# Performance work log

Measured on AMD Instinct MI355X. Metric: run time of the kernel, lower is better.

The kernel has to match this reference:

```python
import jax, jax.numpy as jnp
import numpy as np
import math

N_EMBD = 1024
N_HEAD = 16
B, T = 2, 2048


def new_gelu(x):
    # GPT-2 tanh-approx GELU (matches torch module exactly)
    return 0.5 * x * (1.0 + jnp.tanh(jnp.sqrt(2.0 / jnp.pi) * (x + 0.044715 * x ** 3)))


def layer_norm(x, w, b, eps=1e-5):
    mu = jnp.mean(x, axis=-1, keepdims=True)
    var = jnp.var(x, axis=-1, keepdims=True)
    return (x - mu) * jax.lax.rsqrt(var + eps) * w + b


def setup_inputs() -> dict:
    key = jax.random.key(0)
    ks = jax.random.split(key, 8)
    C = N_EMBD
    s = 0.02
    return {
        "x": jax.random.normal(ks[0], (B, T, C), dtype=jnp.float32),
        "ln1_w": jnp.ones((C,), jnp.float32),
        "ln1_b": jnp.zeros((C,), jnp.float32),
        "attn_w": s * jax.random.normal(ks[1], (C, 3 * C), jnp.float32),
        "attn_b": jnp.zeros((3 * C,), jnp.float32),
        "attn_proj_w": s * jax.random.normal(ks[2], (C, C), jnp.float32),
        "attn_proj_b": jnp.zeros((C,), jnp.float32),
        "ln2_w": jnp.ones((C,), jnp.float32),
        "ln2_b": jnp.zeros((C,), jnp.float32),
        "fc_w": s * jax.random.normal(ks[3], (C, 4 * C), jnp.float32),
        "fc_b": jnp.zeros((4 * C,), jnp.float32),
        "mlp_proj_w": s * jax.random.normal(ks[4], (4 * C, C), jnp.float32),
        "mlp_proj_b": jnp.zeros((C,), jnp.float32),
    }


def block_forward(x, ln1_w, ln1_b, attn_w, attn_b, attn_proj_w, attn_proj_b,
                  ln2_w, ln2_b, fc_w, fc_b, mlp_proj_w, mlp_proj_b):
    Bm, Tm, C = x.shape
    H = N_HEAD
    D = C // H
    # --- self attention (pre-LN) ---
    h = layer_norm(x, ln1_w, ln1_b)
    qkv = h @ attn_w + attn_b  # [B,T,3C]
    q, k, v = jnp.split(qkv, 3, axis=-1)
    q = q.reshape(Bm, Tm, H, D).transpose(0, 2, 1, 3)  # [B,H,T,D]
    k = k.reshape(Bm, Tm, H, D).transpose(0, 2, 1, 3)
    v = v.reshape(Bm, Tm, H, D).transpose(0, 2, 1, 3)
    att = jnp.einsum('bhqd,bhkd->bhqk', q, k) * (1.0 / math.sqrt(D))
    att = jax.nn.softmax(att, axis=-1)  # NOTE: no causal mask in source
    y = jnp.einsum('bhqk,bhkd->bhqd', att, v)
    y = y.transpose(0, 2, 1, 3).reshape(Bm, Tm, C)
    x = x + (y @ attn_proj_w + attn_proj_b)
    # --- MLP ---
    h = layer_norm(x, ln2_w, ln2_b)
    h = new_gelu(h @ fc_w + fc_b)
    x = x + (h @ mlp_proj_w + mlp_proj_b)
    return x


def reference(x, ln1_w, ln1_b, attn_w, attn_b, attn_proj_w, attn_proj_b,
              ln2_w, ln2_b, fc_w, fc_b, mlp_proj_w, mlp_proj_b):
    return block_forward(x, ln1_w, ln1_b, attn_w, attn_b, attn_proj_w, attn_proj_b,
                         ln2_w, ln2_b, fc_w, fc_b, mlp_proj_w, mlp_proj_b)
```

## Files before the change

### kernel.cpp

```cpp
#include <hip/hip_runtime.h>

typedef __attribute__((ext_vector_type(4))) float  f32x4;
typedef __attribute__((ext_vector_type(8))) short  s16x8;
typedef __attribute__((ext_vector_type(4))) short  s16x4;

__device__ __forceinline__ short f2bf(float f) {
    unsigned u = __builtin_bit_cast(unsigned, f);
    u += 0x7fff + ((u >> 16) & 1);
    return (short)(u >> 16);
}

__device__ __forceinline__ void load_lds16(const void* g, void* l) {
    __builtin_amdgcn_global_load_lds(
        (const __attribute__((address_space(1))) unsigned int*)g,
        (__attribute__((address_space(3))) unsigned int*)l, 16, 0, 0);
}

__global__ __launch_bounds__(256) void transpose_cast(const float* __restrict__ W,
                                                      short* __restrict__ Wt,
                                                      int K, int N) {
    __shared__ float t[32][33];
    int n0 = blockIdx.x * 32, k0 = blockIdx.y * 32;
    int tx = threadIdx.x & 31, ty = threadIdx.x >> 5;
#pragma unroll
    for (int i = 0; i < 4; i++)
        t[ty + 8 * i][tx] = W[(size_t)(k0 + ty + 8 * i) * N + n0 + tx];
    __syncthreads();
#pragma unroll
    for (int i = 0; i < 4; i++)
        Wt[(size_t)(n0 + ty + 8 * i) * K + k0 + tx] = f2bf(t[tx][ty + 8 * i]);
}

__global__ __launch_bounds__(256) void vtrans_kernel(const short* __restrict__ qkv,
                                                     short* __restrict__ Vtg) {
    const int T = 2048, C3 = 3072;
    __shared__ short tl[32][33];
    int bh = blockIdx.y >> 1;
    int b = bh >> 4, h = bh & 15;
    int dh = (blockIdx.y & 1) * 32;
    int t0 = blockIdx.x * 32;
    int tx = threadIdx.x & 31, ty = threadIdx.x >> 5;
    const short* src = qkv + (size_t)b * T * C3 + 2048 + h * 64 + dh;
#pragma unroll
    for (int i = 0; i < 4; i++)
        tl[ty + 8 * i][tx] = src[(size_t)(t0 + ty + 8 * i) * C3 + tx];
    __syncthreads();
#pragma unroll
    for (int i = 0; i < 4; i++)
        Vtg[((size_t)bh * 64 + dh + ty + 8 * i) * T + t0 + tx] = tl[tx][ty + 8 * i];
}

__global__ __launch_bounds__(256) void ln_kernel(const float* __restrict__ x,
                                                 const float* __restrict__ w,
                                                 const float* __restrict__ b,
                                                 short* __restrict__ out) {
    int row = blockIdx.x;
    int tid = threadIdx.x;
    const float4 v = ((const float4*)(x + (size_t)row * 1024))[tid];
    float s  = v.x + v.y + v.z + v.w;
    float ss = v.x * v.x + v.y * v.y + v.z * v.z + v.w * v.w;
#pragma unroll
    for (int o = 32; o > 0; o >>= 1) {
        s  += __shfl_down(s, o);
        ss += __shfl_down(ss, o);
    }
    __shared__ float rs[4], rq[4];
    int wave = tid >> 6, lane = tid & 63;
    if (lane == 0) { rs[wave] = s; rq[wave] = ss; }
    __syncthreads();
    float tot = rs[0] + rs[1] + rs[2] + rs[3];
    float tq  = rq[0] + rq[1] + rq[2] + rq[3];
    float mu   = tot * (1.f / 1024.f);
    float var  = tq * (1.f / 1024.f) - mu * mu;
    float rstd = rsqrtf(var + 1e-5f);
    const float4 wv = ((const float4*)w)[tid];
    const float4 bv = ((const float4*)b)[tid];
    s16x4 o;
    o[0] = f2bf((v.x - mu) * rstd * wv.x + bv.x);
    o[1] = f2bf((v.y - mu) * rstd * wv.y + bv.y);
    o[2] = f2bf((v.z - mu) * rstd * wv.z + bv.z);
    o[3] = f2bf((v.w - mu) * rstd * wv.w + bv.w);
    ((s16x4*)(out + (size_t)row * 1024))[tid] = o;
}

template <typename OUT_T, bool GELU, bool RES, bool SCALE_Q>
__global__ __launch_bounds__(256) void gemm_bt(const short* __restrict__ A,
                                               const short* __restrict__ Bt,
                                               const float* __restrict__ bias,
                                               const float* __restrict__ res,
                                               OUT_T* __restrict__ C,
                                               int M, int N, int K) {
    __shared__ __align__(16) short As[128 * 32];
    __shared__ __align__(16) short Bs[128 * 32];
    int tid = threadIdx.x;
    int m0 = blockIdx.y * 128, n0 = blockIdx.x * 128;
    int wave = tid >> 6, lane = tid & 63;
    int wr = wave >> 1, wc = wave & 1;
    int g = lane >> 4, q = lane & 15;
    f32x4 acc[4][4] = {};
    const short* Ab = A + (size_t)m0 * K;
    const short* Bb = Bt + (size_t)n0 * K;
    int srow = tid >> 2;
    int scol = (tid & 3) * 8;
    for (int k0 = 0; k0 < K; k0 += 32) {
        __syncthreads();
        load_lds16(Ab + (size_t)srow * K + k0 + scol, As + tid * 8);
        load_lds16(Ab + (size_t)(srow + 64) * K + k0 + scol, As + 2048 + tid * 8);
        load_lds16(Bb + (size_t)srow * K + k0 + scol, Bs + tid * 8);
        load_lds16(Bb + (size_t)(srow + 64) * K + k0 + scol, Bs + 2048 + tid * 8);
        __syncthreads();
        s16x8 a[4], bf[4];
#pragma unroll
        for (int mi = 0; mi < 4; mi++)
            a[mi] = *(const s16x8*)(As + (wr * 64 + mi * 16 + q) * 32 + g * 8);
#pragma unroll
        for (int ni = 0; ni < 4; ni++)
            bf[ni] = *(const s16x8*)(Bs + (wc * 64 + ni * 16 + q) * 32 + g * 8);
#pragma unroll
        for (int mi = 0; mi < 4; mi++)
#pragma unroll
            for (int ni = 0; ni < 4; ni++)
                acc[mi][ni] = __builtin_amdgcn_mfma_f32_16x16x32_bf16(a[mi], bf[ni], acc[mi][ni], 0, 0, 0);
    }
#pragma unroll
    for (int mi = 0; mi < 4; mi++) {
#pragma unroll
        for (int ni = 0; ni < 4; ni++) {
            int row = m0 + wr * 64 + mi * 16 + g * 4;
            int col = n0 + wc * 64 + ni * 16 + q;
            float bb = bias[col];
#pragma unroll
            for (int r = 0; r < 4; r++) {
                float v = acc[mi][ni][r] + bb;
                if (RES) v += res[(size_t)(row + r) * N + col];
                if (GELU) {
                    float aa = 0.7978845608028654f * (v + 0.044715f * v * v * v);
                    float th = 1.f - 2.f / (__expf(2.f * aa) + 1.f);
                    v = 0.5f * v * (1.f + th);
                }
                if (SCALE_Q && col < 1024) v *= 0.18033688011112042f;
                if constexpr (sizeof(OUT_T) == 2)
                    C[(size_t)(row + r) * N + col] = f2bf(v);
                else
                    C[(size_t)(row + r) * N + col] = v;
            }
        }
    }
}

__global__ __launch_bounds__(256) void attn_kernel(const short* __restrict__ qkv,
                                                   const short* __restrict__ Vtg,
                                                   short* __restrict__ y) {
    const int T = 2048, C3 = 3072;
    int wg = blockIdx.x;
    int mapped = (wg & 7) * 128 + (wg >> 3);
    int bh = mapped >> 5, qt = mapped & 31;
    int b = bh >> 4, h = bh & 15;
    int tid = threadIdx.x, lane = tid & 63, wave = tid >> 6;
    int g = lane >> 4, q = lane & 15;
    const short* base = qkv + (size_t)b * T * C3;

    int qrow = qt * 64 + wave * 16 + q;
    const short* qp = base + (size_t)qrow * C3 + h * 64 + g * 8;
    s16x8 qf0 = *(const s16x8*)qp;
    s16x8 qf1 = *(const s16x8*)(qp + 32);

    __shared__ __align__(16) short Ks[2][64 * 64];
    __shared__ __align__(16) short Vs[2][64 * 64];
    __shared__ __align__(16) short Pl[4][16 * 64];

    int srow = tid >> 3, sc8 = tid & 7;
    const short* ksrc = base + 1024 + h * 64 + (size_t)srow * C3 + ((sc8 ^ (srow & 7)) << 3);
    const short* vsrc = Vtg + ((size_t)bh * 64 + srow) * T + ((sc8 ^ (srow & 7)) << 3);

    auto stage = [&](int bi, int t) {
        const short* kp = ksrc + (size_t)(t * 64) * C3;
        load_lds16(kp, &Ks[bi][tid * 8]);
        load_lds16(kp + (size_t)32 * C3, &Ks[bi][tid * 8 + 2048]);
        const short* vp = vsrc + t * 64;
        load_lds16(vp, &Vs[bi][tid * 8]);
        load_lds16(vp + (size_t)32 * T, &Vs[bi][tid * 8 + 2048]);
    };

    float mst = -INFINITY, lst = 0.f;
    f32x4 accy[4] = {};
    int sw = q & 7;
    int s2 = sw << 1;

    stage(0, 0);
    for (int t = 0; t < 32; ++t) {
        int cur = t & 1;
        __syncthreads();
        if (t < 31) stage(cur ^ 1, t + 1);
        f32x4 sc[4];
#pragma unroll
        for (int n = 0; n < 4; n++) {
            const short* kb = &Ks[cur][(16 * n + q) * 64];
            s16x8 kf0 = *(const s16x8*)(kb + ((g ^ sw) << 3));
            s16x8 kf1 = *(const s16x8*)(kb + (((g + 4) ^ sw) << 3));
            f32x4 z = {};
            z = __builtin_amdgcn_mfma_f32_16x16x32_bf16(kf0, qf0, z, 0, 0, 0);
            sc[n] = __builtin_amdgcn_mfma_f32_16x16x32_bf16(kf1, qf1, z, 0, 0, 0);
        }
        float tm = -INFINITY;
#pragma unroll
        for (int n = 0; n < 4; n++)
#pragma unroll
            for (int r = 0; r < 4; r++) tm = fmaxf(tm, sc[n][r]);
        tm = fmaxf(tm, __shfl_xor(tm, 16));
        tm = fmaxf(tm, __shfl_xor(tm, 32));
        if (!__all(tm <= mst + 8.f)) {
            float mnew = fmaxf(mst, tm);
            float alpha = exp2f(mst - mnew);
            lst *= alpha;
#pragma unroll
            for (int r = 0; r < 4; r++) {
                float ar = __shfl(alpha, 4 * g + r);
#pragma unroll
                for (int n = 0; n < 4; n++) accy[n][r] *= ar;
            }
            mst = mnew;
        }
        float p[4][4];
        float ps = 0.f;
#pragma unroll
        for (int n = 0; n < 4; n++)
#pragma unroll
            for (int r = 0; r < 4; r++) {
                p[n][r] = exp2f(sc[n][r] - mst);
                ps += p[n][r];
            }
        ps += __shfl_xor(ps, 16);
        ps += __shfl_xor(ps, 32);
        lst += ps;
#pragma unroll
        for (int n = 0; n < 4; n++) {
            unsigned w0, w1;
            asm("v_cvt_pk_bf16_f32 %0, %1, %2" : "=v"(w0) : "v"(p[n][0]), "v"(p[n][1]));
            asm("v_cvt_pk_bf16_f32 %0, %1, %2" : "=v"(w1) : "v"(p[n][2]), "v"(p[n][3]));
            unsigned long long pw = (unsigned long long)w0 | ((unsigned long long)w1 << 32);
            *(unsigned long long*)&Pl[wave][q * 64 + (((4 * n + g) ^ s2) << 2)] = pw;
        }
        s16x8 pa0 = *(const s16x8*)&Pl[wave][q * 64 + (((2 * g) ^ s2) << 2)];
        s16x8 pa1 = *(const s16x8*)&Pl[wave][q * 64 + (((8 + 2 * g) ^ s2) << 2)];
#pragma unroll
        for (int n = 0; n < 4; n++) {
            int d = 16 * n + q, vw = d & 7;
            const short* vb = &Vs[cur][d * 64];
            s16x8 v0 = *(const s16x8*)(vb + ((g ^ vw) << 3));
            s16x8 v1 = *(const s16x8*)(vb + (((g + 4) ^ vw) << 3));
            accy[n] = __builtin_amdgcn_mfma_f32_16x16x32_bf16(pa0, v0, accy[n], 0, 0, 0);
            accy[n] = __builtin_amdgcn_mfma_f32_16x16x32_bf16(pa1, v1, accy[n], 0, 0, 0);
        }
    }
    short* yb = y + ((size_t)b * T + qt * 64 + wave * 16) * 1024 + h * 64;
#pragma unroll
    for (int r = 0; r < 4; r++) {
        float linv = 1.f / __shfl(lst, 4 * g + r);
#pragma unroll
        for (int n = 0; n < 4; n++)
            yb[(size_t)(4 * g + r) * 1024 + 16 * n + q] = f2bf(accy[n][r] * linv);
    }
}

extern "C" void kernel_launch(void* const* d_in, const int* in_sizes, int n_in,
                              void* d_out, int out_size, void* d_ws, size_t ws_size,
                              hipStream_t stream) {
    const float* x           = (const float*)d_in[0];
    const float* ln1_w       = (const float*)d_in[1];
    const float* ln1_b       = (const float*)d_in[2];
    const float* attn_w      = (const float*)d_in[3];
    const float* attn_b      = (const float*)d_in[4];
    const float* attn_proj_w = (const float*)d_in[5];
    const float* attn_proj_b = (const float*)d_in[6];
    const float* ln2_w       = (const float*)d_in[7];
    const float* ln2_b       = (const float*)d_in[8];
    const float* fc_w        = (const float*)d_in[9];
    const float* fc_b        = (const float*)d_in[10];
    const float* mlp_proj_w  = (const float*)d_in[11];
    const float* mlp_proj_b  = (const float*)d_in[12];

    const int M = 4096;

    size_t off = 0;
    char* wsb = (char*)d_ws;
    auto alloc = [&](size_t bytes) {
        void* p = wsb + off;
        off += (bytes + 255) & ~(size_t)255;
        return p;
    };
    short* wt_attn  = (short*)alloc(3072ull * 1024 * 2);
    short* wt_proj  = (short*)alloc(1024ull * 1024 * 2);
    short* wt_fc    = (short*)alloc(4096ull * 1024 * 2);
    short* wt_mproj = (short*)alloc(1024ull * 4096 * 2);
    short* h1       = (short*)alloc((size_t)M * 1024 * 2);
    short* qkvb     = (short*)alloc((size_t)M * 3072 * 2);
    short* yb       = (short*)alloc((size_t)M * 1024 * 2);
    float* x1       = (float*)alloc((size_t)M * 1024 * 4);
    short* vtg      = (short*)alloc((size_t)M * 1024 * 2);
    short* h2       = qkvb;

    transpose_cast<<<dim3(3072 / 32, 1024 / 32), 256, 0, stream>>>(attn_w, wt_attn, 1024, 3072);
    transpose_cast<<<dim3(1024 / 32, 1024 / 32), 256, 0, stream>>>(attn_proj_w, wt_proj, 1024, 1024);
    transpose_cast<<<dim3(4096 / 32, 1024 / 32), 256, 0, stream>>>(fc_w, wt_fc, 1024, 4096);
    transpose_cast<<<dim3(1024 / 32, 4096 / 32), 256, 0, stream>>>(mlp_proj_w, wt_mproj, 4096, 1024);

    ln_kernel<<<M, 256, 0, stream>>>(x, ln1_w, ln1_b, h1);
    gemm_bt<short, false, false, true><<<dim3(3072 / 128, M / 128), 256, 0, stream>>>(
        h1, wt_attn, attn_b, nullptr, qkvb, M, 3072, 1024);
    vtrans_kernel<<<dim3(2048 / 32, 64), 256, 0, stream>>>(qkvb, vtg);
    attn_kernel<<<1024, 256, 0, stream>>>(qkvb, vtg, yb);
    gemm_bt<float, false, true, false><<<dim3(1024 / 128, M / 128), 256, 0, stream>>>(
        yb, wt_proj, attn_proj_b, x, x1, M, 1024, 1024);
    ln_kernel<<<M, 256, 0, stream>>>(x1, ln2_w, ln2_b, h1);
    gemm_bt<short, true, false, false><<<dim3(4096 / 128, M / 128), 256, 0, stream>>>(
        h1, wt_fc, fc_b, nullptr, h2, M, 4096, 1024);
    gemm_bt<float, false, true, false><<<dim3(1024 / 128, M / 128), 256, 0, stream>>>(
        h2, wt_mproj, mlp_proj_b, x1, (float*)d_out, M, 1024, 4096);
}
```

Measured before the change: 326.2 us.

## Split-K the MLP down-projection GEMM with a separate reduction kernel

Adds a split-K variant of the bf16 GEMM for the 4096-deep MLP projection. Each K-slice writes fp32 partial tiles to workspace, and a reduction kernel sums them with bias and residual. The aim is more workgroups to fill the GPU on a long-K GEMM that otherwise launches only 256 tiles. In exchange it adds extra global traffic for the partials and an extra kernel launch, and it depends on the workspace being large enough.

```diff
diff --git a/kernel.cpp b/kernel.cpp
--- a/kernel.cpp
+++ b/kernel.cpp
@@ -148,6 +148,84 @@
     }
 }
 
+__global__ __launch_bounds__(256) void gemm_bt_sk(const short* __restrict__ A,
+                                                  const short* __restrict__ Bt,
+                                                  float* __restrict__ part,
+                                                  int M, int N, int K, int Klen) {
+    __shared__ __align__(16) short As[128 * 32];
+    __shared__ __align__(16) short Bs[128 * 32];
+    int tid = threadIdx.x;
+    int m0 = blockIdx.y * 128, n0 = blockIdx.x * 128;
+    int kz = blockIdx.z;
+    int wave = tid >> 6, lane = tid & 63;
+    int wr = wave >> 1, wc = wave & 1;
+    int g = lane >> 4, q = lane & 15;
+    f32x4 acc[4][4] = {};
+    const short* Ab = A + (size_t)m0 * K;
+    const short* Bb = Bt + (size_t)n0 * K;
+    int srow = tid >> 2;
+    int scol = (tid & 3) * 8;
+    int kend = kz * Klen + Klen;
+    for (int k0 = kz * Klen; k0 < kend; k0 += 32) {
+        __syncthreads();
+        load_lds16(Ab + (size_t)srow * K + k0 + scol, As + tid * 8);
+        load_lds16(Ab + (size_t)(srow + 64) * K + k0 + scol, As + 2048 + tid * 8);
+        load_lds16(Bb + (size_t)srow * K + k0 + scol, Bs + tid * 8);
+        load_lds16(Bb + (size_t)(srow + 64) * K + k0 + scol, Bs + 2048 + tid * 8);
+        __syncthreads();
+        s16x8 a[4], bf[4];
+#pragma unroll
+        for (int mi = 0; mi < 4; mi++)
+            a[mi] = *(const s16x8*)(As + (wr * 64 + mi * 16 + q) * 32 + g * 8);
+#pragma unroll
+        for (int ni = 0; ni < 4; ni++)
+            bf[ni] = *(const s16x8*)(Bs + (wc * 64 + ni * 16 + q) * 32 + g * 8);
+#pragma unroll
+        for (int mi = 0; mi < 4; mi++)
+#pragma unroll
+            for (int ni = 0; ni < 4; ni++)
+                acc[mi][ni] = __builtin_amdgcn_mfma_f32_16x16x32_bf16(a[mi], bf[ni], acc[mi][ni], 0, 0, 0);
+    }
+    float* pb = part + (size_t)kz * M * N;
+#pragma unroll
+    for (int mi = 0; mi < 4; mi++) {
+#pragma unroll
+        for (int ni = 0; ni < 4; ni++) {
+            int row = m0 + wr * 64 + mi * 16 + g * 4;
+            int col = n0 + wc * 64 + ni * 16 + q;
+#pragma unroll
+            for (int r = 0; r < 4; r++)
+                pb[(size_t)(row + r) * N + col] = acc[mi][ni][r];
+        }
+    }
+}
+
+template <int SK>
+__global__ __launch_bounds__(256) void reduce_sk(const float* __restrict__ part,
+                                                 const float* __restrict__ bias,
+                                                 const float* __restrict__ res,
+                                                 float* __restrict__ out,
+                                                 int MN, int N) {
+    int tot = MN >> 2;
+    int nb4 = (N >> 2) - 1;
+    for (int i = blockIdx.x * 256 + threadIdx.x; i < tot; i += gridDim.x * 256) {
+        float4 s = ((const float4*)part)[i];
+#pragma unroll
+        for (int k = 1; k < SK; k++) {
+            float4 p = ((const float4*)(part + (size_t)k * MN))[i];
+            s.x += p.x; s.y += p.y; s.z += p.z; s.w += p.w;
+        }
+        float4 bv = ((const float4*)bias)[i & nb4];
+        float4 rv = ((const float4*)res)[i];
+        float4 o;
+        o.x = s.x + bv.x + rv.x;
+        o.y = s.y + bv.y + rv.y;
+        o.z = s.z + bv.z + rv.z;
+        o.w = s.w + bv.w + rv.w;
+        ((float4*)out)[i] = o;
+    }
+}
+
 __global__ __launch_bounds__(256) void attn_kernel(const short* __restrict__ qkv,
                                                    const short* __restrict__ Vtg,
                                                    short* __restrict__ y) {
@@ -300,6 +378,12 @@
     short* vtg      = (short*)alloc((size_t)M * 1024 * 2);
     short* h2       = qkvb;
 
+    size_t base_off = off;
+    int SK = 0;
+    if (ws_size >= base_off + 4ull * M * 1024 * 4) SK = 4;
+    else if (ws_size >= base_off + 2ull * M * 1024 * 4) SK = 2;
+    float* part = (float*)(wsb + base_off);
+
     transpose_cast<<<dim3(3072 / 32, 1024 / 32), 256, 0, stream>>>(attn_w, wt_attn, 1024, 3072);
     transpose_cast<<<dim3(1024 / 32, 1024 / 32), 256, 0, stream>>>(attn_proj_w, wt_proj, 1024, 1024);
     transpose_cast<<<dim3(4096 / 32, 1024 / 32), 256, 0, stream>>>(fc_w, wt_fc, 1024, 4096);
@@ -315,6 +399,17 @@
     ln_kernel<<<M, 256, 0, stream>>>(x1, ln2_w, ln2_b, h1);
     gemm_bt<short, true, false, false><<<dim3(4096 / 128, M / 128), 256, 0, stream>>>(
         h1, wt_fc, fc_b, nullptr, h2, M, 4096, 1024);
-    gemm_bt<float, false, true, false><<<dim3(1024 / 128, M / 128), 256, 0, stream>>>(
-        h2, wt_mproj, mlp_proj_b, x1, (float*)d_out, M, 1024, 4096);
-}
+
+    if (SK == 4) {
+        gemm_bt_sk<<<dim3(1024 / 128, M / 128, 4), 256, 0, stream>>>(
+            h2, wt_mproj, part, M, 1024, 4096, 1024);
+        reduce_sk<4><<<2048, 256, 0, stream>>>(part, mlp_proj_b, x1, (float*)d_out, M * 1024, 1024);
+    } else if (SK == 2) {
+        gemm_bt_sk<<<dim3(1024 / 128, M / 128, 2), 256, 0, stream>>>(
+            h2, wt_mproj, part, M, 1024, 4096, 2048);
+        reduce_sk<2><<<2048, 256, 0, stream>>>(part, mlp_proj_b, x1, (float*)d_out, M * 1024, 1024);
+    } else {
+        gemm_bt<float, false, true, false><<<dim3(1024 / 128, M / 128), 256, 0, stream>>>(
+            h2, wt_mproj, mlp_proj_b, x1, (float*)d_out, M, 1024, 4096);
+    }
+}
```

Measured after the change: 315.5 us. 1.03x faster.
